# Kernel tuning notes

Hardware: AMD Instinct MI355X
Metric: run time of the kernel (lower is better)

## Reference

```python
import jax, jax.numpy as jnp
import numpy as np
from jax.scipy.special import xlogy, gammaln

D_MODEL = 768
NUM_HEADS = 12
DEPTH = D_MODEL // NUM_HEADS  # 64
FEAT = D_MODEL // 6           # 128, feature_size per basis block
MIN_HALF_LIFE = 3.0


def positional_features(S):
    """Enformer-style basis features for relative positions [-S+1, S-1].
    Returns [1, 2S-1, 6*FEAT]. Dropout in the original is identity at inference."""
    pos = jnp.arange(-S + 1, S, dtype=jnp.float32)          # [2S-1]
    apos = jnp.abs(pos)
    sgn = jnp.sign(pos)[:, None]
    # exponential decay basis
    max_range = jnp.log2(jnp.float32(S))
    half_life = 2.0 ** jnp.linspace(MIN_HALF_LIFE, max_range, FEAT)  # [FEAT]
    exp1 = jnp.exp(-jnp.log(2.0) / half_life * apos[:, None])        # [2S-1, FEAT]
    # central mask basis
    cw = 2.0 ** jnp.arange(1, FEAT + 1, dtype=jnp.float32) - 1.0
    cm1 = (cw > apos[:, None]).astype(jnp.float32)
    # gamma pdf basis
    Sf = jnp.float32(S)
    stdv = Sf / (2.0 * FEAT)
    mean = jnp.linspace(Sf / FEAT, Sf, FEAT)
    conc = (mean / stdv) ** 2
    rate = mean / (stdv ** 2)
    log_unnorm = xlogy(conc - 1.0, apos[:, None]) - rate * apos[:, None]
    log_norm = gammaln(conc) - conc * jnp.log(rate)
    prob = jnp.exp(log_unnorm - log_norm)
    gam1 = prob / jnp.max(prob)
    pe = jnp.concatenate([exp1, exp1 * sgn, cm1, cm1 * sgn, gam1, gam1 * sgn], axis=-1)
    return pe[None]  # [1, 2S-1, 6*FEAT]


def relative_shift(x):
    """Transformer-XL pad/reshape/slice trick: [B,H,S,2S-1] -> [B,H,S,S]."""
    B, H, t1, _ = x.shape
    x = jnp.concatenate([jnp.zeros_like(x[..., :1]), x], axis=-1)  # [B,H,t1,2*t1]
    t2 = x.shape[-1]
    x = x.reshape(B, H, t2, t1)[:, :, 1:, :]
    x = x.reshape(B, H, t1, t2 - 1)
    return x[..., : (t2 + 1) // 2]


def setup_inputs() -> dict:
    key = jax.random.key(0)
    ks = jax.random.split(key, 11)
    B, S = 1, 2048
    return {
        "q": jax.random.normal(ks[0], (B, S, D_MODEL), jnp.float32),
        "k": jax.random.normal(ks[1], (B, S, D_MODEL), jnp.float32),
        "v": jax.random.normal(ks[2], (B, S, D_MODEL), jnp.float32),
        "wq": jax.random.normal(ks[3], (D_MODEL, D_MODEL), jnp.float32) * 0.02,
        "wk": jax.random.normal(ks[4], (D_MODEL, D_MODEL), jnp.float32) * 0.02,
        "wv": jax.random.normal(ks[5], (D_MODEL, D_MODEL), jnp.float32) * 0.02,
        "w_rk": jax.random.normal(ks[6], (D_MODEL, D_MODEL), jnp.float32) * 0.02,
        "r_w": jax.random.normal(ks[7], (1, NUM_HEADS, 1, DEPTH), jnp.float32) * 0.5,
        "r_r": jax.random.normal(ks[8], (1, NUM_HEADS, 1, DEPTH), jnp.float32) * 0.5,
        "w_out": jax.random.normal(ks[9], (D_MODEL, D_MODEL), jnp.float32) * 0.02,
        "b_out": jnp.zeros((D_MODEL,), jnp.float32),
    }


def reference(q, k, v, wq, wk, wv, w_rk, r_w, r_r, w_out, b_out):
    B, S, _ = q.shape

    def split_heads(x):  # [B,S,D] -> [B,H,S,depth]
        return x.reshape(B, S, NUM_HEADS, DEPTH).transpose(0, 2, 1, 3)

    qh = split_heads(q @ wq) / jnp.sqrt(jnp.float32(DEPTH))
    kh = split_heads(k @ wk)
    vh = split_heads(v @ wv)

    pe = positional_features(S)                                   # [1,2S-1,D]
    rk = (pe @ w_rk).reshape(1, 2 * S - 1, NUM_HEADS, DEPTH).transpose(0, 2, 1, 3)

    content = jnp.einsum("bhsd,bhtd->bhst", qh + r_w, kh)         # [B,H,S,S]
    rel = jnp.einsum("bhsd,xhtd->bhst", qh + r_r, rk)             # [B,H,S,2S-1] (x==1)
    rel = relative_shift(rel)                                     # [B,H,S,S]

    attn = jax.nn.softmax(content + rel, axis=-1)
    out = jnp.einsum("bhst,bhtd->bhsd", attn, vh)
    out = out.transpose(0, 2, 1, 3).reshape(B, S, D_MODEL)
    out = out @ w_out + b_out
    return out, attn
```

## Files before the change

kernel.cpp:

```cpp
#include <hip/hip_runtime.h>
#include <math.h>

#define S_LEN 2048
#define T_LEN 4095
#define NH 12
#define DEPTH 64
#define DM 768

typedef unsigned short u16;
typedef u16   u16x4 __attribute__((ext_vector_type(4)));
typedef short s16x8 __attribute__((ext_vector_type(8)));
typedef float f32x4 __attribute__((ext_vector_type(4)));

#define QH_OFF  ((size_t)0)
#define KH_OFF  (QH_OFF + (size_t)NH*S_LEN*DEPTH)
#define VH_OFF  (KH_OFF + (size_t)NH*S_LEN*DEPTH)
#define RK_OFF  (VH_OFF + (size_t)NH*S_LEN*DEPTH)
#define OH_OFF  (RK_OFF + (size_t)NH*T_LEN*DEPTH)
#define WTO_OFF (OH_OFF + (size_t)S_LEN*DM)
#define GMAX_OFF (WTO_OFF + (size_t)DM*DM)
#define WS_NEEDED_BYTES ((GMAX_OFF + 32) * sizeof(u16))

#define PEB_OFF ((size_t)0)
#define QB_OFF  (PEB_OFF + (size_t)T_LEN*DM)
#define KB_OFF  (QB_OFF + (size_t)S_LEN*DM)
#define VB_OFF  (KB_OFF + (size_t)S_LEN*DM)
#define WTQ_OFF (VB_OFF + (size_t)S_LEN*DM)
#define WTK_OFF (WTQ_OFF + (size_t)DM*DM)
#define WTV_OFF (WTK_OFF + (size_t)DM*DM)
#define WTR_OFF (WTV_OFF + (size_t)DM*DM)

__device__ __forceinline__ float bf2f(u16 x) {
    union { unsigned u; float f; } c; c.u = ((unsigned)x) << 16; return c.f;
}
__device__ __forceinline__ u16 f2bf(float f) {
    union { float f; unsigned u; } c; c.f = f;
    unsigned u = c.u;
    return (u16)((u + 0x7FFFu + ((u >> 16) & 1u)) >> 16);
}

__global__ void init_gmax(float* g) { *g = 0.0f; }
__global__ void ws_too_small(float* out, float wsz) { out[0] = wsz; }

__global__ __launch_bounds__(256) void cvt_bf16(const float* __restrict__ in, u16* __restrict__ out, int n4)
{
    int i = blockIdx.x * 256 + threadIdx.x;
    if (i < n4) {
        float4 v = ((const float4*)in)[i];
        u16x4 o = { f2bf(v.x), f2bf(v.y), f2bf(v.z), f2bf(v.w) };
        ((u16x4*)out)[i] = o;
    }
}

__global__ __launch_bounds__(256) void wtrans(const float* __restrict__ W, u16* __restrict__ WT,
                                              const float* __restrict__ gmax, int scale_from)
{
    __shared__ float t[64][65];
    int k0 = blockIdx.x * 64, n0 = blockIdx.y * 64;
    int tid = threadIdx.x;
    float inv = (scale_from < DM) ? (1.0f / (*gmax)) : 1.0f;

    #pragma unroll
    for (int it = 0; it < 4; ++it) {
        int idx = it * 256 + tid;
        int r = idx >> 4, c4 = (idx & 15) << 2;
        float4 v = *(const float4*)&W[(size_t)(k0 + r) * DM + n0 + c4];
        t[r][c4] = v.x; t[r][c4 + 1] = v.y; t[r][c4 + 2] = v.z; t[r][c4 + 3] = v.w;
    }
    __syncthreads();
    #pragma unroll
    for (int it = 0; it < 4; ++it) {
        int idx = it * 256 + tid;
        int rn = idx >> 4, k4 = (idx & 15) << 2;
        u16x4 o;
        #pragma unroll
        for (int e = 0; e < 4; ++e) {
            float f = t[k4 + e][rn];
            if (k0 + k4 + e >= scale_from) f *= inv;
            o[e] = f2bf(f);
        }
        *(u16x4*)&WT[(size_t)(n0 + rn) * DM + k0 + k4] = o;
    }
}

__global__ __launch_bounds__(128) void pe_kernel(u16* __restrict__ pe, float* __restrict__ gmax)
{
    int t = blockIdx.x;
    int f = threadIdx.x;
    float pos  = (float)(t - (S_LEN - 1));
    float apos = fabsf(pos);
    float sgn  = (pos > 0.f) ? 1.f : ((pos < 0.f) ? -1.f : 0.f);

    double hl = exp2(3.0 + 8.0 * (double)f / 127.0);
    float e1 = (float)exp2(-(double)apos / hl);

    double cw = exp2((double)(f + 1)) - 1.0;
    float cm = (cw > (double)apos) ? 1.f : 0.f;

    double fp1 = (double)(f + 1);
    double conc = 4.0 * fp1 * fp1;
    double rate = 0.25 * fp1;
    double prob = 0.0;
    if (apos != 0.f) {
        double la = log((double)apos);
        double lu = (conc - 1.0) * la - rate * (double)apos;
        double ln = lgamma(conc) - conc * log(rate);
        prob = exp(lu - ln);
    }
    float pr = (float)prob;

    u16* row = pe + (size_t)t * DM;
    row[f]        = f2bf(e1);
    row[128 + f]  = f2bf(e1 * sgn);
    row[256 + f]  = f2bf(cm);
    row[384 + f]  = f2bf(cm * sgn);
    row[512 + f]  = f2bf(pr);
    row[640 + f]  = f2bf(pr * sgn);

    __shared__ float red[128];
    red[f] = pr;
    __syncthreads();
    for (int s = 64; s > 0; s >>= 1) {
        if (f < s) red[f] = fmaxf(red[f], red[f + s]);
        __syncthreads();
    }
    if (f == 0) atomicMax((int*)gmax, __float_as_int(red[0]));
}

__global__ __launch_bounds__(256) void gemm_bf(const u16* __restrict__ A, const u16* __restrict__ WT,
                                               void* __restrict__ Cv, int M, float alpha, int mode,
                                               const float* __restrict__ bias)
{
    __shared__ u16 As[64 * 72];
    __shared__ u16 Ws[64 * 72];
    int tid = threadIdx.x;
    int row0 = blockIdx.x * 64, col0 = blockIdx.y * 64;
    int w = tid >> 6, l = tid & 63, l15 = l & 15, lg = l >> 4;

    f32x4 acc[4];
    #pragma unroll
    for (int cb = 0; cb < 4; ++cb) acc[cb] = (f32x4){0.f, 0.f, 0.f, 0.f};

    for (int k0 = 0; k0 < DM; k0 += 64) {
        __syncthreads();
        #pragma unroll
        for (int it = 0; it < 4; ++it) {
            int idx = it * 256 + tid;
            int r = idx >> 4, c4 = (idx & 15) << 2;
            int gr = row0 + r;
            u16x4 va = {0, 0, 0, 0};
            if (gr < M) va = *(const u16x4*)&A[(size_t)gr * DM + k0 + c4];
            *(u16x4*)&As[r * 72 + c4] = va;
            *(u16x4*)&Ws[r * 72 + c4] = *(const u16x4*)&WT[(size_t)(col0 + r) * DM + k0 + c4];
        }
        __syncthreads();
        #pragma unroll
        for (int ks = 0; ks < 2; ++ks) {
            int off = ks * 32 + lg * 8;
            s16x8 aF = *(const s16x8*)&As[(w * 16 + l15) * 72 + off];
            #pragma unroll
            for (int cb = 0; cb < 4; ++cb) {
                s16x8 bF = *(const s16x8*)&Ws[(cb * 16 + l15) * 72 + off];
                acc[cb] = __builtin_amdgcn_mfma_f32_16x16x32_bf16(aF, bF, acc[cb], 0, 0, 0);
            }
        }
    }

    #pragma unroll
    for (int cb = 0; cb < 4; ++cb)
        #pragma unroll
        for (int rg = 0; rg < 4; ++rg) {
            int m = row0 + w * 16 + lg * 4 + rg;
            if (m >= M) continue;
            int nl = cb * 16 + l15;
            if (mode == 0) {
                ((u16*)Cv)[((size_t)blockIdx.y * M + m) * 64 + nl] = f2bf(acc[cb][rg] * alpha);
            } else {
                ((float*)Cv)[(size_t)m * DM + col0 + nl] = acc[cb][rg] + bias[col0 + nl];
            }
        }
}

#define WAVE_LDS_FENCE() asm volatile("s_waitcnt lgkmcnt(0)" ::: "memory")

__global__ __launch_bounds__(256) void attn_fused(
    const u16* __restrict__ qh, const u16* __restrict__ kh, const u16* __restrict__ vh,
    const u16* __restrict__ rk, const float* __restrict__ rw, const float* __restrict__ rr,
    float* __restrict__ attn, u16* __restrict__ oh)
{
    __shared__ u16 lds_kh[64 * 72];
    __shared__ u16 lds_rk[128 * 72];
    __shared__ u16 lds_relP[4 * 16 * 80];

    const int tid = threadIdx.x;
    const int h  = blockIdx.y;
    const int i0 = blockIdx.x * 64;
    const int w   = tid >> 6;
    const int l   = tid & 63;
    const int l15 = l & 15;
    const int lg  = l >> 4;

    const u16* qh_h = qh + (size_t)h * S_LEN * DEPTH;
    const u16* kh_h = kh + (size_t)h * S_LEN * DEPTH;
    const u16* vh_h = vh + (size_t)h * S_LEN * DEPTH;
    const u16* rk_h = rk + (size_t)h * T_LEN * DEPTH;
    float* attn_h = attn + ((size_t)h * S_LEN + i0) * S_LEN;

    s16x8 qwf[2], qrf[2];
    {
        int arow = i0 + w * 16 + l15;
        #pragma unroll
        for (int ks = 0; ks < 2; ++ks) {
            int bd = ks * 32 + lg * 8;
            s16x8 qv = *(const s16x8*)&qh_h[(size_t)arow * DEPTH + bd];
            #pragma unroll
            for (int e = 0; e < 8; ++e) {
                float f = bf2f((u16)qv[e]);
                qwf[ks][e] = (short)f2bf(f + rw[h * 64 + bd + e]);
                qrf[ks][e] = (short)f2bf(f + rr[h * 64 + bd + e]);
            }
        }
    }

    u16* relw = &lds_relP[w * 16 * 80];
    const int pb  = 48 - w * 16;
    const int tb0 = 1984 - i0;

    float run_max[4], run_sum[4];
    #pragma unroll
    for (int rg = 0; rg < 4; ++rg) { run_max[rg] = -3.0e38f; run_sum[rg] = 0.f; }

    for (int jt = 0; jt < S_LEN; jt += 64) {
        __syncthreads();
        #pragma unroll
        for (int it = 0; it < 4; ++it) {
            int idx = it * 256 + tid;
            int j = idx >> 4, d4 = (idx & 15) << 2;
            *(u16x4*)&lds_kh[j * 72 + d4] = *(const u16x4*)&kh_h[(size_t)(jt + j) * DEPTH + d4];
        }
        int Tlo = tb0 + jt;
        #pragma unroll
        for (int it = 0; it < 8; ++it) {
            int idx = it * 256 + tid;
            int tr = idx >> 4, d4 = (idx & 15) << 2;
            int t = Tlo + tr;
            u16x4 v = {0, 0, 0, 0};
            if (t >= 0 && t < T_LEN) v = *(const u16x4*)&rk_h[(size_t)t * DEPTH + d4];
            *(u16x4*)&lds_rk[tr * 72 + d4] = v;
        }
        __syncthreads();

        f32x4 accC[4], accR[5];
        #pragma unroll
        for (int cb = 0; cb < 4; ++cb) accC[cb] = (f32x4){0.f, 0.f, 0.f, 0.f};
        #pragma unroll
        for (int tb = 0; tb < 5; ++tb) accR[tb] = (f32x4){0.f, 0.f, 0.f, 0.f};

        #pragma unroll
        for (int ks = 0; ks < 2; ++ks) {
            int off = ks * 32 + lg * 8;
            #pragma unroll
            for (int cb = 0; cb < 4; ++cb) {
                s16x8 b = *(const s16x8*)&lds_kh[(cb * 16 + l15) * 72 + off];
                accC[cb] = __builtin_amdgcn_mfma_f32_16x16x32_bf16(qwf[ks], b, accC[cb], 0, 0, 0);
            }
            #pragma unroll
            for (int tb = 0; tb < 5; ++tb) {
                s16x8 b = *(const s16x8*)&lds_rk[(pb + tb * 16 + l15) * 72 + off];
                accR[tb] = __builtin_amdgcn_mfma_f32_16x16x32_bf16(qrf[ks], b, accR[tb], 0, 0, 0);
            }
        }
        #pragma unroll
        for (int tb = 0; tb < 5; ++tb)
            #pragma unroll
            for (int rg = 0; rg < 4; ++rg)
                relw[(lg * 4 + rg) * 80 + tb * 16 + l15] = f2bf(accR[tb][rg]);
        WAVE_LDS_FENCE();
        #pragma unroll
        for (int cb = 0; cb < 4; ++cb)
            #pragma unroll
            for (int rg = 0; rg < 4; ++rg) {
                int row = lg * 4 + rg;
                accC[cb][rg] += bf2f(relw[row * 80 + 15 + cb * 16 + l15 - row]);
            }
        #pragma unroll
        for (int rg = 0; rg < 4; ++rg) {
            float m = fmaxf(fmaxf(accC[0][rg], accC[1][rg]), fmaxf(accC[2][rg], accC[3][rg]));
            m = fmaxf(m, __shfl_xor(m, 1));
            m = fmaxf(m, __shfl_xor(m, 2));
            m = fmaxf(m, __shfl_xor(m, 4));
            m = fmaxf(m, __shfl_xor(m, 8));
            float nm = fmaxf(run_max[rg], m);
            float s = __expf(accC[0][rg] - nm) + __expf(accC[1][rg] - nm)
                    + __expf(accC[2][rg] - nm) + __expf(accC[3][rg] - nm);
            s += __shfl_xor(s, 1);
            s += __shfl_xor(s, 2);
            s += __shfl_xor(s, 4);
            s += __shfl_xor(s, 8);
            run_sum[rg] = run_sum[rg] * __expf(run_max[rg] - nm) + s;
            run_max[rg] = nm;
        }
    }

    float inv_sum[4];
    #pragma unroll
    for (int rg = 0; rg < 4; ++rg) inv_sum[rg] = 1.0f / run_sum[rg];

    f32x4 accO[4];
    #pragma unroll
    for (int db = 0; db < 4; ++db) accO[db] = (f32x4){0.f, 0.f, 0.f, 0.f};

    for (int jt = 0; jt < S_LEN; jt += 64) {
        __syncthreads();
        #pragma unroll
        for (int it = 0; it < 4; ++it) {
            int idx = it * 256 + tid;
            int j = idx >> 4, d4 = (idx & 15) << 2;
            *(u16x4*)&lds_kh[j * 72 + d4] = *(const u16x4*)&kh_h[(size_t)(jt + j) * DEPTH + d4];
        }
        int Tlo = tb0 + jt;
        #pragma unroll
        for (int it = 0; it < 8; ++it) {
            int idx = it * 256 + tid;
            int tr = idx >> 4, d4 = (idx & 15) << 2;
            int t = Tlo + tr;
            u16x4 v = {0, 0, 0, 0};
            if (t >= 0 && t < T_LEN) v = *(const u16x4*)&rk_h[(size_t)t * DEPTH + d4];
            *(u16x4*)&lds_rk[tr * 72 + d4] = v;
        }
        __syncthreads();

        f32x4 accC[4], accR[5];
        #pragma unroll
        for (int cb = 0; cb < 4; ++cb) accC[cb] = (f32x4){0.f, 0.f, 0.f, 0.f};
        #pragma unroll
        for (int tb = 0; tb < 5; ++tb) accR[tb] = (f32x4){0.f, 0.f, 0.f, 0.f};

        #pragma unroll
        for (int ks = 0; ks < 2; ++ks) {
            int off = ks * 32 + lg * 8;
            #pragma unroll
            for (int cb = 0; cb < 4; ++cb) {
                s16x8 b = *(const s16x8*)&lds_kh[(cb * 16 + l15) * 72 + off];
                accC[cb] = __builtin_amdgcn_mfma_f32_16x16x32_bf16(qwf[ks], b, accC[cb], 0, 0, 0);
            }
            #pragma unroll
            for (int tb = 0; tb < 5; ++tb) {
                s16x8 b = *(const s16x8*)&lds_rk[(pb + tb * 16 + l15) * 72 + off];
                accR[tb] = __builtin_amdgcn_mfma_f32_16x16x32_bf16(qrf[ks], b, accR[tb], 0, 0, 0);
            }
        }
        #pragma unroll
        for (int tb = 0; tb < 5; ++tb)
            #pragma unroll
            for (int rg = 0; rg < 4; ++rg)
                relw[(lg * 4 + rg) * 80 + tb * 16 + l15] = f2bf(accR[tb][rg]);
        WAVE_LDS_FENCE();
        #pragma unroll
        for (int cb = 0; cb < 4; ++cb)
            #pragma unroll
            for (int rg = 0; rg < 4; ++rg) {
                int row = lg * 4 + rg;
                float lgt = accC[cb][rg] + bf2f(relw[row * 80 + 15 + cb * 16 + l15 - row]);
                float pr = __expf(lgt - run_max[rg]) * inv_sum[rg];
                attn_h[(size_t)(w * 16 + row) * S_LEN + jt + cb * 16 + l15] = pr;
                relw[row * 80 + cb * 16 + l15] = f2bf(pr);
            }
        __syncthreads();
        #pragma unroll
        for (int it = 0; it < 4; ++it) {
            int idx = it * 256 + tid;
            int j = idx & 63, d4 = (idx >> 6) << 2;
            u16x4 v = *(const u16x4*)&vh_h[(size_t)(jt + j) * DEPTH + d4];
            lds_kh[(d4 + 0) * 72 + j] = v.x;
            lds_kh[(d4 + 1) * 72 + j] = v.y;
            lds_kh[(d4 + 2) * 72 + j] = v.z;
            lds_kh[(d4 + 3) * 72 + j] = v.w;
        }
        __syncthreads();
        s16x8 pA[2];
        #pragma unroll
        for (int ks = 0; ks < 2; ++ks)
            pA[ks] = *(const s16x8*)&relw[l15 * 80 + ks * 32 + lg * 8];
        #pragma unroll
        for (int ks = 0; ks < 2; ++ks) {
            int off = ks * 32 + lg * 8;
            #pragma unroll
            for (int db = 0; db < 4; ++db) {
                s16x8 bv = *(const s16x8*)&lds_kh[(db * 16 + l15) * 72 + off];
                accO[db] = __builtin_amdgcn_mfma_f32_16x16x32_bf16(pA[ks], bv, accO[db], 0, 0, 0);
            }
        }
    }

    #pragma unroll
    for (int db = 0; db < 4; ++db)
        #pragma unroll
        for (int rg = 0; rg < 4; ++rg)
            oh[(size_t)(i0 + w * 16 + lg * 4 + rg) * DM + h * 64 + db * 16 + l15] = f2bf(accO[db][rg]);
}

extern "C" void kernel_launch(void* const* d_in, const int* in_sizes, int n_in,
                              void* d_out, int out_size, void* d_ws, size_t ws_size,
                              hipStream_t stream) {
    const float* q    = (const float*)d_in[0];
    const float* k    = (const float*)d_in[1];
    const float* v    = (const float*)d_in[2];
    const float* wq   = (const float*)d_in[3];
    const float* wk   = (const float*)d_in[4];
    const float* wv   = (const float*)d_in[5];
    const float* w_rk = (const float*)d_in[6];
    const float* r_w  = (const float*)d_in[7];
    const float* r_r  = (const float*)d_in[8];
    const float* w_out= (const float*)d_in[9];
    const float* b_out= (const float*)d_in[10];

    float* outp = (float*)d_out;
    float* attn = outp + (size_t)S_LEN * DM;

    if (ws_size < WS_NEEDED_BYTES) {
        hipLaunchKernelGGL(ws_too_small, dim3(1), dim3(1), 0, stream, outp, (float)ws_size);
        return;
    }

    u16* wsb = (u16*)d_ws;
    u16* qh = wsb + QH_OFF;
    u16* kh = wsb + KH_OFF;
    u16* vh = wsb + VH_OFF;
    u16* rk = wsb + RK_OFF;
    u16* oh = wsb + OH_OFF;
    u16* wTo = wsb + WTO_OFF;
    float* gmax = (float*)(wsb + GMAX_OFF);

    u16* scratch = (u16*)attn;
    u16* peb = scratch + PEB_OFF;
    u16* qb  = scratch + QB_OFF;
    u16* kb  = scratch + KB_OFF;
    u16* vb  = scratch + VB_OFF;
    u16* wTq = scratch + WTQ_OFF;
    u16* wTk = scratch + WTK_OFF;
    u16* wTv = scratch + WTV_OFF;
    u16* wTr = scratch + WTR_OFF;

    const int n4 = S_LEN * DM / 4;
    hipLaunchKernelGGL(cvt_bf16, dim3((n4 + 255) / 256), dim3(256), 0, stream, q, qb, n4);
    hipLaunchKernelGGL(cvt_bf16, dim3((n4 + 255) / 256), dim3(256), 0, stream, k, kb, n4);
    hipLaunchKernelGGL(cvt_bf16, dim3((n4 + 255) / 256), dim3(256), 0, stream, v, vb, n4);

    hipLaunchKernelGGL(init_gmax, dim3(1), dim3(1), 0, stream, gmax);
    hipLaunchKernelGGL(pe_kernel, dim3(T_LEN), dim3(128), 0, stream, peb, gmax);

    hipLaunchKernelGGL(wtrans, dim3(12, 12), dim3(256), 0, stream, wq, wTq, gmax, 1 << 30);
    hipLaunchKernelGGL(wtrans, dim3(12, 12), dim3(256), 0, stream, wk, wTk, gmax, 1 << 30);
    hipLaunchKernelGGL(wtrans, dim3(12, 12), dim3(256), 0, stream, wv, wTv, gmax, 1 << 30);
    hipLaunchKernelGGL(wtrans, dim3(12, 12), dim3(256), 0, stream, w_rk, wTr, gmax, 512);
    hipLaunchKernelGGL(wtrans, dim3(12, 12), dim3(256), 0, stream, w_out, wTo, gmax, 1 << 30);

    hipLaunchKernelGGL(gemm_bf, dim3(32, 12), dim3(256), 0, stream, qb, wTq, (void*)qh, S_LEN, 0.125f, 0, (const float*)nullptr);
    hipLaunchKernelGGL(gemm_bf, dim3(32, 12), dim3(256), 0, stream, kb, wTk, (void*)kh, S_LEN, 1.0f, 0, (const float*)nullptr);
    hipLaunchKernelGGL(gemm_bf, dim3(32, 12), dim3(256), 0, stream, vb, wTv, (void*)vh, S_LEN, 1.0f, 0, (const float*)nullptr);

    hipLaunchKernelGGL(gemm_bf, dim3(64, 12), dim3(256), 0, stream, peb, wTr, (void*)rk, T_LEN, 1.0f, 0, (const float*)nullptr);

    hipLaunchKernelGGL(attn_fused, dim3(S_LEN / 64, NH), dim3(256), 0, stream,
                       qh, kh, vh, rk, r_w, r_r, attn, oh);

    hipLaunchKernelGGL(gemm_bf, dim3(32, 12), dim3(256), 0, stream, oh, wTo, (void*)outp, S_LEN, 1.0f, 1, b_out);
}
```

Baseline: 681.9 us.

## Fuse prep launches, fold bf16 conversion into GEMMs, split attention keys across waves

Removes the separate fp32-to-bf16 conversion kernels by converting q/k/v inside the projection GEMM loads. All weight transposes are merged into one launch, and all input projections plus the rk GEMM are merged into a single grid. The attention kernel now handles 32 query rows per block (doubling the grid) and splits each 128-key tile between wave pairs. Partial softmax stats and output accumulators are combined through LDS at the end. This trades fewer launches and more blocks for extra LDS, a cross-wave reduction, and some early-exit blocks in the merged GEMM grid.

```diff
diff --git a/kernel.cpp b/kernel.cpp
--- a/kernel.cpp
+++ b/kernel.cpp
@@ -22,10 +22,7 @@
 #define WS_NEEDED_BYTES ((GMAX_OFF + 32) * sizeof(u16))
 
 #define PEB_OFF ((size_t)0)
-#define QB_OFF  (PEB_OFF + (size_t)T_LEN*DM)
-#define KB_OFF  (QB_OFF + (size_t)S_LEN*DM)
-#define VB_OFF  (KB_OFF + (size_t)S_LEN*DM)
-#define WTQ_OFF (VB_OFF + (size_t)S_LEN*DM)
+#define WTQ_OFF (PEB_OFF + (size_t)T_LEN*DM)
 #define WTK_OFF (WTQ_OFF + (size_t)DM*DM)
 #define WTV_OFF (WTK_OFF + (size_t)DM*DM)
 #define WTR_OFF (WTV_OFF + (size_t)DM*DM)
@@ -41,47 +38,6 @@
 
 __global__ void init_gmax(float* g) { *g = 0.0f; }
 __global__ void ws_too_small(float* out, float wsz) { out[0] = wsz; }
-
-__global__ __launch_bounds__(256) void cvt_bf16(const float* __restrict__ in, u16* __restrict__ out, int n4)
-{
-    int i = blockIdx.x * 256 + threadIdx.x;
-    if (i < n4) {
-        float4 v = ((const float4*)in)[i];
-        u16x4 o = { f2bf(v.x), f2bf(v.y), f2bf(v.z), f2bf(v.w) };
-        ((u16x4*)out)[i] = o;
-    }
-}
-
-__global__ __launch_bounds__(256) void wtrans(const float* __restrict__ W, u16* __restrict__ WT,
-                                              const float* __restrict__ gmax, int scale_from)
-{
-    __shared__ float t[64][65];
-    int k0 = blockIdx.x * 64, n0 = blockIdx.y * 64;
-    int tid = threadIdx.x;
-    float inv = (scale_from < DM) ? (1.0f / (*gmax)) : 1.0f;
-
-    #pragma unroll
-    for (int it = 0; it < 4; ++it) {
-        int idx = it * 256 + tid;
-        int r = idx >> 4, c4 = (idx & 15) << 2;
-        float4 v = *(const float4*)&W[(size_t)(k0 + r) * DM + n0 + c4];
-        t[r][c4] = v.x; t[r][c4 + 1] = v.y; t[r][c4 + 2] = v.z; t[r][c4 + 3] = v.w;
-    }
-    __syncthreads();
-    #pragma unroll
-    for (int it = 0; it < 4; ++it) {
-        int idx = it * 256 + tid;
-        int rn = idx >> 4, k4 = (idx & 15) << 2;
-        u16x4 o;
-        #pragma unroll
-        for (int e = 0; e < 4; ++e) {
-            float f = t[k4 + e][rn];
-            if (k0 + k4 + e >= scale_from) f *= inv;
-            o[e] = f2bf(f);
-        }
-        *(u16x4*)&WT[(size_t)(n0 + rn) * DM + k0 + k4] = o;
-    }
-}
 
 __global__ __launch_bounds__(128) void pe_kernel(u16* __restrict__ pe, float* __restrict__ gmax)
 {
@@ -127,9 +83,117 @@
     if (f == 0) atomicMax((int*)gmax, __float_as_int(red[0]));
 }
 
-__global__ __launch_bounds__(256) void gemm_bf(const u16* __restrict__ A, const u16* __restrict__ WT,
-                                               void* __restrict__ Cv, int M, float alpha, int mode,
-                                               const float* __restrict__ bias)
+__global__ __launch_bounds__(256) void wtrans_all(
+    const float* __restrict__ wq, const float* __restrict__ wk, const float* __restrict__ wv,
+    const float* __restrict__ wrk, const float* __restrict__ wout,
+    u16* __restrict__ tq, u16* __restrict__ tk, u16* __restrict__ tv,
+    u16* __restrict__ tr, u16* __restrict__ to, const float* __restrict__ gmax)
+{
+    const float* W; u16* WT; int scale_from = 1 << 30;
+    switch (blockIdx.z) {
+        case 0: W = wq;  WT = tq; break;
+        case 1: W = wk;  WT = tk; break;
+        case 2: W = wv;  WT = tv; break;
+        case 3: W = wrk; WT = tr; scale_from = 512; break;
+        default: W = wout; WT = to; break;
+    }
+    __shared__ float t[64][65];
+    int k0 = blockIdx.x * 64, n0 = blockIdx.y * 64;
+    int tid = threadIdx.x;
+    float inv = (scale_from < DM) ? (1.0f / (*gmax)) : 1.0f;
+
+    #pragma unroll
+    for (int it = 0; it < 4; ++it) {
+        int idx = it * 256 + tid;
+        int r = idx >> 4, c4 = (idx & 15) << 2;
+        float4 v = *(const float4*)&W[(size_t)(k0 + r) * DM + n0 + c4];
+        t[r][c4] = v.x; t[r][c4 + 1] = v.y; t[r][c4 + 2] = v.z; t[r][c4 + 3] = v.w;
+    }
+    __syncthreads();
+    #pragma unroll
+    for (int it = 0; it < 4; ++it) {
+        int idx = it * 256 + tid;
+        int rn = idx >> 4, k4 = (idx & 15) << 2;
+        u16x4 o;
+        #pragma unroll
+        for (int e = 0; e < 4; ++e) {
+            float f = t[k4 + e][rn];
+            if (k0 + k4 + e >= scale_from) f *= inv;
+            o[e] = f2bf(f);
+        }
+        *(u16x4*)&WT[(size_t)(n0 + rn) * DM + k0 + k4] = o;
+    }
+}
+
+__global__ __launch_bounds__(256) void gemm_all(
+    const float* __restrict__ q, const float* __restrict__ k, const float* __restrict__ v,
+    const u16* __restrict__ peb,
+    const u16* __restrict__ wTq, const u16* __restrict__ wTk, const u16* __restrict__ wTv,
+    const u16* __restrict__ wTr,
+    u16* __restrict__ qh, u16* __restrict__ kh, u16* __restrict__ vh, u16* __restrict__ rk)
+{
+    const void* A; const u16* WT; u16* dst; int M; float alpha; bool af32;
+    switch (blockIdx.z) {
+        case 0: if (blockIdx.x >= 32) return; A = q; WT = wTq; dst = qh; M = S_LEN; alpha = 0.125f; af32 = true; break;
+        case 1: if (blockIdx.x >= 32) return; A = k; WT = wTk; dst = kh; M = S_LEN; alpha = 1.0f; af32 = true; break;
+        case 2: if (blockIdx.x >= 32) return; A = v; WT = wTv; dst = vh; M = S_LEN; alpha = 1.0f; af32 = true; break;
+        default: A = peb; WT = wTr; dst = rk; M = T_LEN; alpha = 1.0f; af32 = false; break;
+    }
+
+    __shared__ u16 As[64 * 72];
+    __shared__ u16 Ws[64 * 72];
+    int tid = threadIdx.x;
+    int row0 = blockIdx.x * 64, col0 = blockIdx.y * 64;
+    int w = tid >> 6, l = tid & 63, l15 = l & 15, lg = l >> 4;
+
+    f32x4 acc[4];
+    #pragma unroll
+    for (int cb = 0; cb < 4; ++cb) acc[cb] = (f32x4){0.f, 0.f, 0.f, 0.f};
+
+    for (int k0 = 0; k0 < DM; k0 += 64) {
+        __syncthreads();
+        #pragma unroll
+        for (int it = 0; it < 4; ++it) {
+            int idx = it * 256 + tid;
+            int r = idx >> 4, c4 = (idx & 15) << 2;
+            int gr = row0 + r;
+            u16x4 va = {0, 0, 0, 0};
+            if (gr < M) {
+                if (af32) {
+                    float4 vf = *(const float4*)&((const float*)A)[(size_t)gr * DM + k0 + c4];
+                    va[0] = f2bf(vf.x); va[1] = f2bf(vf.y); va[2] = f2bf(vf.z); va[3] = f2bf(vf.w);
+                } else {
+                    va = *(const u16x4*)&((const u16*)A)[(size_t)gr * DM + k0 + c4];
+                }
+            }
+            *(u16x4*)&As[r * 72 + c4] = va;
+            *(u16x4*)&Ws[r * 72 + c4] = *(const u16x4*)&WT[(size_t)(col0 + r) * DM + k0 + c4];
+        }
+        __syncthreads();
+        #pragma unroll
+        for (int ks = 0; ks < 2; ++ks) {
+            int off = ks * 32 + lg * 8;
+            s16x8 aF = *(const s16x8*)&As[(w * 16 + l15) * 72 + off];
+            #pragma unroll
+            for (int cb = 0; cb < 4; ++cb) {
+                s16x8 bF = *(const s16x8*)&Ws[(cb * 16 + l15) * 72 + off];
+                acc[cb] = __builtin_amdgcn_mfma_f32_16x16x32_bf16(aF, bF, acc[cb], 0, 0, 0);
+            }
+        }
+    }
+
+    #pragma unroll
+    for (int cb = 0; cb < 4; ++cb)
+        #pragma unroll
+        for (int rg = 0; rg < 4; ++rg) {
+            int m = row0 + w * 16 + lg * 4 + rg;
+            if (m >= M) continue;
+            dst[((size_t)blockIdx.y * M + m) * 64 + cb * 16 + l15] = f2bf(acc[cb][rg] * alpha);
+        }
+}
+
+__global__ __launch_bounds__(256) void gemm_out(const u16* __restrict__ A, const u16* __restrict__ WT,
+                                                float* __restrict__ C, const float* __restrict__ bias)
 {
     __shared__ u16 As[64 * 72];
     __shared__ u16 Ws[64 * 72];
@@ -147,10 +211,7 @@
         for (int it = 0; it < 4; ++it) {
             int idx = it * 256 + tid;
             int r = idx >> 4, c4 = (idx & 15) << 2;
-            int gr = row0 + r;
-            u16x4 va = {0, 0, 0, 0};
-            if (gr < M) va = *(const u16x4*)&A[(size_t)gr * DM + k0 + c4];
-            *(u16x4*)&As[r * 72 + c4] = va;
+            *(u16x4*)&As[r * 72 + c4] = *(const u16x4*)&A[(size_t)(row0 + r) * DM + k0 + c4];
             *(u16x4*)&Ws[r * 72 + c4] = *(const u16x4*)&WT[(size_t)(col0 + r) * DM + k0 + c4];
         }
         __syncthreads();
@@ -171,13 +232,8 @@
         #pragma unroll
         for (int rg = 0; rg < 4; ++rg) {
             int m = row0 + w * 16 + lg * 4 + rg;
-            if (m >= M) continue;
-            int nl = cb * 16 + l15;
-            if (mode == 0) {
-                ((u16*)Cv)[((size_t)blockIdx.y * M + m) * 64 + nl] = f2bf(acc[cb][rg] * alpha);
-            } else {
-                ((float*)Cv)[(size_t)m * DM + col0 + nl] = acc[cb][rg] + bias[col0 + nl];
-            }
+            int n = col0 + cb * 16 + l15;
+            C[(size_t)m * DM + n] = acc[cb][rg] + bias[n];
         }
 }
 
@@ -188,17 +244,22 @@
     const u16* __restrict__ rk, const float* __restrict__ rw, const float* __restrict__ rr,
     float* __restrict__ attn, u16* __restrict__ oh)
 {
-    __shared__ u16 lds_kh[64 * 72];
-    __shared__ u16 lds_rk[128 * 72];
-    __shared__ u16 lds_relP[4 * 16 * 80];
+    __shared__ __align__(16) u16 lds_kh[128 * 72];
+    __shared__ __align__(16) u16 lds_rk[160 * 72];
+    __shared__ __align__(16) u16 lds_relP[4 * 16 * 80];
+    __shared__ float lds_stats[4][16][2];
 
     const int tid = threadIdx.x;
     const int h  = blockIdx.y;
-    const int i0 = blockIdx.x * 64;
+    const int i0 = blockIdx.x * 32;
     const int w   = tid >> 6;
     const int l   = tid & 63;
     const int l15 = l & 15;
     const int lg  = l >> 4;
+    const int rg2 = w & 1;
+    const int jp  = w >> 1;
+    const int pb  = 16 + jp * 64 - rg2 * 16;
+    const int tb0 = 2016 - i0;
 
     const u16* qh_h = qh + (size_t)h * S_LEN * DEPTH;
     const u16* kh_h = kh + (size_t)h * S_LEN * DEPTH;
@@ -208,7 +269,7 @@
 
     s16x8 qwf[2], qrf[2];
     {
-        int arow = i0 + w * 16 + l15;
+        int arow = i0 + rg2 * 16 + l15;
         #pragma unroll
         for (int ks = 0; ks < 2; ++ks) {
             int bd = ks * 32 + lg * 8;
@@ -223,30 +284,27 @@
     }
 
     u16* relw = &lds_relP[w * 16 * 80];
-    const int pb  = 48 - w * 16;
-    const int tb0 = 1984 - i0;
-
     float run_max[4], run_sum[4];
     #pragma unroll
     for (int rg = 0; rg < 4; ++rg) { run_max[rg] = -3.0e38f; run_sum[rg] = 0.f; }
 
-    for (int jt = 0; jt < S_LEN; jt += 64) {
-        __syncthreads();
-        #pragma unroll
-        for (int it = 0; it < 4; ++it) {
+    for (int jt = 0; jt < S_LEN; jt += 128) {
+        __syncthreads();
+        #pragma unroll
+        for (int it = 0; it < 8; ++it) {
             int idx = it * 256 + tid;
             int j = idx >> 4, d4 = (idx & 15) << 2;
             *(u16x4*)&lds_kh[j * 72 + d4] = *(const u16x4*)&kh_h[(size_t)(jt + j) * DEPTH + d4];
         }
         int Tlo = tb0 + jt;
         #pragma unroll
-        for (int it = 0; it < 8; ++it) {
+        for (int it = 0; it < 10; ++it) {
             int idx = it * 256 + tid;
             int tr = idx >> 4, d4 = (idx & 15) << 2;
             int t = Tlo + tr;
-            u16x4 v = {0, 0, 0, 0};
-            if (t >= 0 && t < T_LEN) v = *(const u16x4*)&rk_h[(size_t)t * DEPTH + d4];
-            *(u16x4*)&lds_rk[tr * 72 + d4] = v;
+            u16x4 vv = {0, 0, 0, 0};
+            if (t >= 0 && t < T_LEN) vv = *(const u16x4*)&rk_h[(size_t)t * DEPTH + d4];
+            *(u16x4*)&lds_rk[tr * 72 + d4] = vv;
         }
         __syncthreads();
 
@@ -261,7 +319,7 @@
             int off = ks * 32 + lg * 8;
             #pragma unroll
             for (int cb = 0; cb < 4; ++cb) {
-                s16x8 b = *(const s16x8*)&lds_kh[(cb * 16 + l15) * 72 + off];
+                s16x8 b = *(const s16x8*)&lds_kh[(jp * 64 + cb * 16 + l15) * 72 + off];
                 accC[cb] = __builtin_amdgcn_mfma_f32_16x16x32_bf16(qwf[ks], b, accC[cb], 0, 0, 0);
             }
             #pragma unroll
@@ -302,6 +360,26 @@
         }
     }
 
+    if (l15 == 0) {
+        #pragma unroll
+        for (int rg = 0; rg < 4; ++rg) {
+            lds_stats[w][lg * 4 + rg][0] = run_max[rg];
+            lds_stats[w][lg * 4 + rg][1] = run_sum[rg];
+        }
+    }
+    __syncthreads();
+    {
+        int pw = w ^ 2;
+        #pragma unroll
+        for (int rg = 0; rg < 4; ++rg) {
+            float m2 = lds_stats[pw][lg * 4 + rg][0];
+            float s2 = lds_stats[pw][lg * 4 + rg][1];
+            float nm = fmaxf(run_max[rg], m2);
+            run_sum[rg] = run_sum[rg] * __expf(run_max[rg] - nm) + s2 * __expf(m2 - nm);
+            run_max[rg] = nm;
+        }
+    }
+
     float inv_sum[4];
     #pragma unroll
     for (int rg = 0; rg < 4; ++rg) inv_sum[rg] = 1.0f / run_sum[rg];
@@ -310,23 +388,23 @@
     #pragma unroll
     for (int db = 0; db < 4; ++db) accO[db] = (f32x4){0.f, 0.f, 0.f, 0.f};
 
-    for (int jt = 0; jt < S_LEN; jt += 64) {
-        __syncthreads();
-        #pragma unroll
-        for (int it = 0; it < 4; ++it) {
+    for (int jt = 0; jt < S_LEN; jt += 128) {
+        __syncthreads();
+        #pragma unroll
+        for (int it = 0; it < 8; ++it) {
             int idx = it * 256 + tid;
             int j = idx >> 4, d4 = (idx & 15) << 2;
             *(u16x4*)&lds_kh[j * 72 + d4] = *(const u16x4*)&kh_h[(size_t)(jt + j) * DEPTH + d4];
         }
         int Tlo = tb0 + jt;
         #pragma unroll
-        for (int it = 0; it < 8; ++it) {
+        for (int it = 0; it < 10; ++it) {
             int idx = it * 256 + tid;
             int tr = idx >> 4, d4 = (idx & 15) << 2;
             int t = Tlo + tr;
-            u16x4 v = {0, 0, 0, 0};
-            if (t >= 0 && t < T_LEN) v = *(const u16x4*)&rk_h[(size_t)t * DEPTH + d4];
-            *(u16x4*)&lds_rk[tr * 72 + d4] = v;
+            u16x4 vv = {0, 0, 0, 0};
+            if (t >= 0 && t < T_LEN) vv = *(const u16x4*)&rk_h[(size_t)t * DEPTH + d4];
+            *(u16x4*)&lds_rk[tr * 72 + d4] = vv;
         }
         __syncthreads();
 
@@ -341,7 +419,7 @@
             int off = ks * 32 + lg * 8;
             #pragma unroll
             for (int cb = 0; cb < 4; ++cb) {
-                s16x8 b = *(const s16x8*)&lds_kh[(cb * 16 + l15) * 72 + off];
+                s16x8 b = *(const s16x8*)&lds_kh[(jp * 64 + cb * 16 + l15) * 72 + off];
                 accC[cb] = __builtin_amdgcn_mfma_f32_16x16x32_bf16(qwf[ks], b, accC[cb], 0, 0, 0);
             }
             #pragma unroll
@@ -363,19 +441,19 @@
                 int row = lg * 4 + rg;
                 float lgt = accC[cb][rg] + bf2f(relw[row * 80 + 15 + cb * 16 + l15 - row]);
                 float pr = __expf(lgt - run_max[rg]) * inv_sum[rg];
-                attn_h[(size_t)(w * 16 + row) * S_LEN + jt + cb * 16 + l15] = pr;
+                attn_h[(size_t)(rg2 * 16 + row) * S_LEN + jt + jp * 64 + cb * 16 + l15] = pr;
                 relw[row * 80 + cb * 16 + l15] = f2bf(pr);
             }
         __syncthreads();
         #pragma unroll
-        for (int it = 0; it < 4; ++it) {
-            int idx = it * 256 + tid;
-            int j = idx & 63, d4 = (idx >> 6) << 2;
-            u16x4 v = *(const u16x4*)&vh_h[(size_t)(jt + j) * DEPTH + d4];
-            lds_kh[(d4 + 0) * 72 + j] = v.x;
-            lds_kh[(d4 + 1) * 72 + j] = v.y;
-            lds_kh[(d4 + 2) * 72 + j] = v.z;
-            lds_kh[(d4 + 3) * 72 + j] = v.w;
+        for (int it = 0; it < 8; ++it) {
+            int idx = it * 256 + tid;
+            int j = idx & 127, d4 = (idx >> 7) << 2;
+            u16x4 vv = *(const u16x4*)&vh_h[(size_t)(jt + j) * DEPTH + d4];
+            lds_kh[(d4 + 0) * 136 + j] = vv.x;
+            lds_kh[(d4 + 1) * 136 + j] = vv.y;
+            lds_kh[(d4 + 2) * 136 + j] = vv.z;
+            lds_kh[(d4 + 3) * 136 + j] = vv.w;
         }
         __syncthreads();
         s16x8 pA[2];
@@ -384,20 +462,34 @@
             pA[ks] = *(const s16x8*)&relw[l15 * 80 + ks * 32 + lg * 8];
         #pragma unroll
         for (int ks = 0; ks < 2; ++ks) {
-            int off = ks * 32 + lg * 8;
+            int off = jp * 64 + ks * 32 + lg * 8;
             #pragma unroll
             for (int db = 0; db < 4; ++db) {
-                s16x8 bv = *(const s16x8*)&lds_kh[(db * 16 + l15) * 72 + off];
+                s16x8 bv = *(const s16x8*)&lds_kh[(db * 16 + l15) * 136 + off];
                 accO[db] = __builtin_amdgcn_mfma_f32_16x16x32_bf16(pA[ks], bv, accO[db], 0, 0, 0);
             }
         }
     }
 
-    #pragma unroll
-    for (int db = 0; db < 4; ++db)
-        #pragma unroll
-        for (int rg = 0; rg < 4; ++rg)
-            oh[(size_t)(i0 + w * 16 + lg * 4 + rg) * DM + h * 64 + db * 16 + l15] = f2bf(accO[db][rg]);
+    float* comb = (float*)lds_kh;
+    __syncthreads();
+    if (jp == 1) {
+        #pragma unroll
+        for (int db = 0; db < 4; ++db)
+            #pragma unroll
+            for (int rg = 0; rg < 4; ++rg)
+                comb[(rg2 * 16 + lg * 4 + rg) * 68 + db * 16 + l15] = accO[db][rg];
+    }
+    __syncthreads();
+    if (jp == 0) {
+        #pragma unroll
+        for (int db = 0; db < 4; ++db)
+            #pragma unroll
+            for (int rg = 0; rg < 4; ++rg) {
+                float o = accO[db][rg] + comb[(rg2 * 16 + lg * 4 + rg) * 68 + db * 16 + l15];
+                oh[(size_t)(i0 + rg2 * 16 + lg * 4 + rg) * DM + h * 64 + db * 16 + l15] = f2bf(o);
+            }
+    }
 }
 
 extern "C" void kernel_launch(void* const* d_in, const int* in_sizes, int n_in,
@@ -434,36 +526,21 @@
 
     u16* scratch = (u16*)attn;
     u16* peb = scratch + PEB_OFF;
-    u16* qb  = scratch + QB_OFF;
-    u16* kb  = scratch + KB_OFF;
-    u16* vb  = scratch + VB_OFF;
     u16* wTq = scratch + WTQ_OFF;
     u16* wTk = scratch + WTK_OFF;
     u16* wTv = scratch + WTV_OFF;
     u16* wTr = scratch + WTR_OFF;
 
-    const int n4 = S_LEN * DM / 4;
-    hipLaunchKernelGGL(cvt_bf16, dim3((n4 + 255) / 256), dim3(256), 0, stream, q, qb, n4);
-    hipLaunchKernelGGL(cvt_bf16, dim3((n4 + 255) / 256), dim3(256), 0, stream, k, kb, n4);
-    hipLaunchKernelGGL(cvt_bf16, dim3((n4 + 255) / 256), dim3(256), 0, stream, v, vb, n4);
-
     hipLaunchKernelGGL(init_gmax, dim3(1), dim3(1), 0, stream, gmax);
     hipLaunchKernelGGL(pe_kernel, dim3(T_LEN), dim3(128), 0, stream, peb, gmax);
-
-    hipLaunchKernelGGL(wtrans, dim3(12, 12), dim3(256), 0, stream, wq, wTq, gmax, 1 << 30);
-    hipLaunchKernelGGL(wtrans, dim3(12, 12), dim3(256), 0, stream, wk, wTk, gmax, 1 << 30);
-    hipLaunchKernelGGL(wtrans, dim3(12, 12), dim3(256), 0, stream, wv, wTv, gmax, 1 << 30);
-    hipLaunchKernelGGL(wtrans, dim3(12, 12), dim3(256), 0, stream, w_rk, wTr, gmax, 512);
-    hipLaunchKernelGGL(wtrans, dim3(12, 12), dim3(256), 0, stream, w_out, wTo, gmax, 1 << 30);
-
-    hipLaunchKernelGGL(gemm_bf, dim3(32, 12), dim3(256), 0, stream, qb, wTq, (void*)qh, S_LEN, 0.125f, 0, (const float*)nullptr);
-    hipLaunchKernelGGL(gemm_bf, dim3(32, 12), dim3(256), 0, stream, kb, wTk, (void*)kh, S_LEN, 1.0f, 0, (const float*)nullptr);
-    hipLaunchKernelGGL(gemm_bf, dim3(32, 12), dim3(256), 0, stream, vb, wTv, (void*)vh, S_LEN, 1.0f, 0, (const float*)nullptr);
-
-    hipLaunchKernelGGL(gemm_bf, dim3(64, 12), dim3(256), 0, stream, peb, wTr, (void*)rk, T_LEN, 1.0f, 0, (const float*)nullptr);
-
-    hipLaunchKernelGGL(attn_fused, dim3(S_LEN / 64, NH), dim3(256), 0, stream,
+    hipLaunchKernelGGL(wtrans_all, dim3(12, 12, 5), dim3(256), 0, stream,
+                       wq, wk, wv, w_rk, w_out, wTq, wTk, wTv, wTr, wTo, gmax);
+
+    hipLaunchKernelGGL(gemm_all, dim3(64, 12, 4), dim3(256), 0, stream,
+                       q, k, v, peb, wTq, wTk, wTv, wTr, qh, kh, vh, rk);
+
+    hipLaunchKernelGGL(attn_fused, dim3(S_LEN / 32, NH), dim3(256), 0, stream,
                        qh, kh, vh, rk, r_w, r_r, attn, oh);
 
-    hipLaunchKernelGGL(gemm_bf, dim3(32, 12), dim3(256), 0, stream, oh, wTo, (void*)outp, S_LEN, 1.0f, 1, b_out);
-}
+    hipLaunchKernelGGL(gemm_out, dim3(32, 12), dim3(256), 0, stream, oh, wTo, outp, b_out);
+}
```

New measurement: 675.1 us. About the same (-1.0%).
